# Kernel optimization log

Hardware: AMD Instinct MI355X
Metric: run time of the kernel (lower is better)

Reference implementation:

```python
import jax, jax.numpy as jnp
import numpy as np

N_NODES = 100000
N_EDGES = 1600000
DIMS = [64, 64, 64, 32]  # in -> hid -> hid -> out


def setup_inputs() -> dict:
    key = jax.random.key(0)
    ks = jax.random.split(key, 12)
    features = jax.random.normal(ks[0], (N_NODES, DIMS[0]), dtype=jnp.float32)
    edge_weights = jax.random.uniform(ks[1], (N_EDGES,), dtype=jnp.float32)
    src = jax.random.randint(ks[2], (N_EDGES,), 0, N_NODES, dtype=jnp.int32)
    dst = jax.random.randint(ks[3], (N_EDGES,), 0, N_NODES, dtype=jnp.int32)
    def lin(kw, kb, i, o):
        s = 1.0 / np.sqrt(i)
        W = jax.random.uniform(kw, (i, o), minval=-s, maxval=s, dtype=jnp.float32)
        b = jax.random.uniform(kb, (o,), minval=-s, maxval=s, dtype=jnp.float32)
        return W, b
    W1, b1 = lin(ks[4], ks[5], DIMS[0], DIMS[1])
    W2, b2 = lin(ks[6], ks[7], DIMS[1], DIMS[2])
    Wp, bp = lin(ks[8], ks[9], DIMS[2], DIMS[3])
    return {"features": features, "edge_weights": edge_weights, "src": src,
            "dst": dst, "W1": W1, "b1": b1, "W2": W2, "b2": b2,
            "Wp": Wp, "bp": bp}


def _graph_conv(x, src, dst, ew, W, b, norm_src, norm_dst):
    # DGL GraphConv, norm='both', with edge weights:
    # h = D_in^{-1/2} * A_w * (D_out^{-1/2} * x) @ W + b
    h = x * norm_src[:, None]
    msg = h[src] * ew[:, None]                      # [E, d] gather + edge-weight
    agg = jax.ops.segment_sum(msg, dst, num_segments=N_NODES)  # scatter-sum
    agg = agg * norm_dst[:, None]
    return agg @ W + b


def reference(features, edge_weights, src, dst, W1, b1, W2, b2, Wp, bp):
    ones = jnp.ones((N_EDGES,), dtype=features.dtype)
    out_deg = jax.ops.segment_sum(ones, src, num_segments=N_NODES)
    in_deg = jax.ops.segment_sum(ones, dst, num_segments=N_NODES)
    norm_src = jnp.power(jnp.clip(out_deg, 1.0, None), -0.5)
    norm_dst = jnp.power(jnp.clip(in_deg, 1.0, None), -0.5)

    x = jax.nn.relu(_graph_conv(features, src, dst, edge_weights, W1, b1, norm_src, norm_dst))
    x = jax.nn.relu(_graph_conv(x, src, dst, edge_weights, W2, b2, norm_src, norm_dst))
    x = _graph_conv(x, src, dst, edge_weights, Wp, bp, norm_src, norm_dst)
    return x
```

## Files before the change

### kernel.cpp

```cpp
#include <hip/hip_runtime.h>

#define N_NODES 100000
#define N_EDGES 1600000
#define NB_SCAN 391
#define NSLICE 64
#define SLICE_E 25000
#define NBUCK 4
#define BUCK_N 25000
#define BUCK_W 12500

__device__ __forceinline__ unsigned short f2bf(float f) {
    unsigned int u = __float_as_uint(f);
    return (unsigned short)((u + 0x7FFFu + ((u >> 16) & 1u)) >> 16);
}
__device__ __forceinline__ float bf2f(unsigned short b) {
    return __uint_as_float(((unsigned int)b) << 16);
}


template <bool RANK>
__global__ void __launch_bounds__(512) count_kernel(
        const int* __restrict__ ids,
        unsigned short* __restrict__ slicecnt,
        unsigned short* __restrict__ rank16) {
    __shared__ unsigned int cnt[BUCK_W];
    int s = blockIdx.x >> 2;
    int b = blockIdx.x & 3;
    int b0 = b * BUCK_N;
    for (int w = threadIdx.x; w < BUCK_W; w += 512) cnt[w] = 0;
    __syncthreads();
    int base = s * SLICE_E;
    for (int i = threadIdx.x; i < SLICE_E; i += 512) {
        int e = base + i;
        int id = ids[e] - b0;
        if ((unsigned)id < (unsigned)BUCK_N) {
            unsigned int shift = (id & 1) * 16;
            unsigned int old = atomicAdd(&cnt[id >> 1], 1u << shift);
            if (RANK) rank16[e] = (unsigned short)((old >> shift) & 0xFFFFu);
        }
    }
    __syncthreads();
    unsigned int* row = (unsigned int*)(slicecnt + (size_t)s * N_NODES) + b * BUCK_W;
    for (int w = threadIdx.x; w < BUCK_W; w += 512) row[w] = cnt[w];
}

__global__ void scan_slices_kernel(unsigned short* __restrict__ scd,
                                   const unsigned short* __restrict__ scs,
                                   int* __restrict__ deg_int,
                                   float* __restrict__ ndq,
                                   float* __restrict__ norm_src) {
    int n = blockIdx.x * blockDim.x + threadIdx.x;
    if (n >= N_NODES) return;
    unsigned int tot = 0;
    for (int s = 0; s < NSLICE; ++s) {
        size_t idx = (size_t)s * N_NODES + n;
        unsigned int c = scd[idx];
        scd[idx] = (unsigned short)tot;
        tot += c;
    }
    deg_int[n] = (int)tot;
    ndq[n] = rsqrtf(fmaxf((float)tot, 1.0f)) * (1.0f / 32767.0f);
    unsigned int so = 0;
    for (int s = 0; s < NSLICE; ++s) so += scs[(size_t)s * N_NODES + n];
    norm_src[n] = rsqrtf(fmaxf((float)so, 1.0f));
}


__global__ void block_sum_kernel(const int* __restrict__ deg_in, int* __restrict__ block_sums) {
    __shared__ int sdata[256];
    int t = threadIdx.x;
    int n = blockIdx.x * 256 + t;
    int v = (n < N_NODES) ? deg_in[n] : 0;
    sdata[t] = v;
    __syncthreads();
    for (int off = 128; off > 0; off >>= 1) {
        if (t < off) sdata[t] += sdata[t + off];
        __syncthreads();
    }
    if (t == 0) block_sums[blockIdx.x] = sdata[0];
}

__global__ void scan_blocks_kernel(const int* __restrict__ block_sums, int* __restrict__ block_off) {
    __shared__ int part[512];
    int t = threadIdx.x;
    int v = (t < NB_SCAN) ? block_sums[t] : 0;
    part[t] = v;
    __syncthreads();
    for (int off = 1; off < 512; off <<= 1) {
        int u = (t >= off) ? part[t - off] : 0;
        __syncthreads();
        part[t] += u;
        __syncthreads();
    }
    if (t < NB_SCAN) block_off[t] = part[t] - v;
}

__global__ void scatter_rowptr_kernel(const int* __restrict__ deg_in,
                                      const int* __restrict__ block_off,
                                      int* __restrict__ row_ptr) {
    __shared__ int part[256];
    int t = threadIdx.x;
    int n = blockIdx.x * 256 + t;
    int v = (n < N_NODES) ? deg_in[n] : 0;
    part[t] = v;
    __syncthreads();
    for (int off = 1; off < 256; off <<= 1) {
        int u = (t >= off) ? part[t - off] : 0;
        __syncthreads();
        part[t] += u;
        __syncthreads();
    }
    int excl = part[t] - v + block_off[blockIdx.x];
    if (n < N_NODES) row_ptr[n] = excl;
    if (n == N_NODES - 1) row_ptr[N_NODES] = excl + v;
}


__global__ void fill_kernel(const int* __restrict__ src, const int* __restrict__ dst,
                            const float* __restrict__ ew,
                            const int* __restrict__ row_ptr,
                            const unsigned short* __restrict__ sliceoff,
                            const unsigned short* __restrict__ rank16,
                            unsigned int* __restrict__ epack) {
    int i = blockIdx.x * blockDim.x + threadIdx.x;
    int stride = gridDim.x * blockDim.x;
    for (int e = i; e < N_EDGES; e += stride) {
        int s = src[e], d = dst[e];
        int sl = e / SLICE_E;
        int slot = row_ptr[d] + (int)sliceoff[(size_t)sl * N_NODES + d] + (int)rank16[e];
        unsigned int q = (unsigned int)(ew[e] * 32767.0f + 0.5f);
        epack[slot] = ((unsigned int)s << 15) | q;
    }
}


template <int BM, int DOUT, bool BIAS_RELU>
__global__ void __launch_bounds__(256) matmul_kernel(
        const float* __restrict__ x, const float* __restrict__ W,
        const float* __restrict__ bin, const float* __restrict__ ns,
        unsigned short* __restrict__ h) {
    constexpr int S = 65;
    constexpr int CG = DOUT / 4;
    __shared__ float Xs[BM * S];
    __shared__ float Ws[64 * DOUT];
    int tid = threadIdx.x;
    int n0 = blockIdx.x * BM;

    for (int i = tid; i < 16 * DOUT; i += 256)
        ((float4*)Ws)[i] = ((const float4*)W)[i];

    float4 bv4;
    if (BIAS_RELU) bv4 = ((const float4*)bin)[tid & 15];
    int c0 = (tid & 15) * 4;
    for (int r = tid >> 4; r < BM; r += 16) {
        int n = n0 + r;
        int nc = n < N_NODES ? n : N_NODES - 1;
        float4 v = ((const float4*)(x + (size_t)nc * 64))[tid & 15];
        if (BIAS_RELU) {
            v.x = fmaxf(v.x + bv4.x, 0.0f);
            v.y = fmaxf(v.y + bv4.y, 0.0f);
            v.z = fmaxf(v.z + bv4.z, 0.0f);
            v.w = fmaxf(v.w + bv4.w, 0.0f);
        }
        Xs[r * S + c0]     = v.x;
        Xs[r * S + c0 + 1] = v.y;
        Xs[r * S + c0 + 2] = v.z;
        Xs[r * S + c0 + 3] = v.w;
    }
    __syncthreads();

    int cg = tid % CG;
    int ng = tid / CG;
    float acc[4][4];
#pragma unroll
    for (int i = 0; i < 4; ++i)
#pragma unroll
        for (int j = 0; j < 4; ++j) acc[i][j] = 0.0f;

#pragma unroll 16
    for (int k = 0; k < 64; ++k) {
        float4 wk = *(const float4*)(&Ws[k * DOUT + cg * 4]);
        float xk[4];
#pragma unroll
        for (int i = 0; i < 4; ++i) xk[i] = Xs[(ng * 4 + i) * S + k];
#pragma unroll
        for (int i = 0; i < 4; ++i) {
            acc[i][0] = fmaf(xk[i], wk.x, acc[i][0]);
            acc[i][1] = fmaf(xk[i], wk.y, acc[i][1]);
            acc[i][2] = fmaf(xk[i], wk.z, acc[i][2]);
            acc[i][3] = fmaf(xk[i], wk.w, acc[i][3]);
        }
    }

#pragma unroll
    for (int i = 0; i < 4; ++i) {
        int n = n0 + ng * 4 + i;
        if (n < N_NODES) {
            float nsv = ns[n];
            ushort4 o;
            o.x = f2bf(acc[i][0] * nsv); o.y = f2bf(acc[i][1] * nsv);
            o.z = f2bf(acc[i][2] * nsv); o.w = f2bf(acc[i][3] * nsv);
            *(ushort4*)(&h[(size_t)n * DOUT + cg * 4]) = o;
        }
    }
}


template <int D, bool FINAL>
__global__ void __launch_bounds__(256) csr_agg_kernel(
        const int* __restrict__ row_ptr,
        const unsigned int* __restrict__ epack,
        const unsigned short* __restrict__ h,
        const float* __restrict__ ndq,
        const float* __restrict__ bias, float* __restrict__ out) {
    int tid = blockIdx.x * blockDim.x + threadIdx.x;
    int stride = gridDim.x * blockDim.x;
    int lane = threadIdx.x & (D - 1);
    int node0 = tid / D;
    int nstride = stride / D;
    const unsigned short* hl = h + lane;
    for (int n = node0; n < N_NODES; n += nstride) {
        int s = row_ptr[n];
        int e = row_ptr[n + 1];
        float a0 = 0.f, a1 = 0.f, a2 = 0.f, a3 = 0.f;
        float a4 = 0.f, a5 = 0.f, a6 = 0.f, a7 = 0.f;
        int i = s;
        for (; i + 7 < e; i += 8) {
            unsigned int p0 = epack[i],     p1 = epack[i + 1], p2 = epack[i + 2], p3 = epack[i + 3];
            unsigned int p4 = epack[i + 4], p5 = epack[i + 5], p6 = epack[i + 6], p7 = epack[i + 7];
            float h0 = bf2f(hl[(size_t)(p0 >> 15) * D]);
            float h1 = bf2f(hl[(size_t)(p1 >> 15) * D]);
            float h2 = bf2f(hl[(size_t)(p2 >> 15) * D]);
            float h3 = bf2f(hl[(size_t)(p3 >> 15) * D]);
            float h4 = bf2f(hl[(size_t)(p4 >> 15) * D]);
            float h5 = bf2f(hl[(size_t)(p5 >> 15) * D]);
            float h6 = bf2f(hl[(size_t)(p6 >> 15) * D]);
            float h7 = bf2f(hl[(size_t)(p7 >> 15) * D]);
            a0 = fmaf((float)(p0 & 32767u), h0, a0);
            a1 = fmaf((float)(p1 & 32767u), h1, a1);
            a2 = fmaf((float)(p2 & 32767u), h2, a2);
            a3 = fmaf((float)(p3 & 32767u), h3, a3);
            a4 = fmaf((float)(p4 & 32767u), h4, a4);
            a5 = fmaf((float)(p5 & 32767u), h5, a5);
            a6 = fmaf((float)(p6 & 32767u), h6, a6);
            a7 = fmaf((float)(p7 & 32767u), h7, a7);
        }
        for (; i + 3 < e; i += 4) {
            unsigned int p0 = epack[i], p1 = epack[i + 1], p2 = epack[i + 2], p3 = epack[i + 3];
            a0 = fmaf((float)(p0 & 32767u), bf2f(hl[(size_t)(p0 >> 15) * D]), a0);
            a1 = fmaf((float)(p1 & 32767u), bf2f(hl[(size_t)(p1 >> 15) * D]), a1);
            a2 = fmaf((float)(p2 & 32767u), bf2f(hl[(size_t)(p2 >> 15) * D]), a2);
            a3 = fmaf((float)(p3 & 32767u), bf2f(hl[(size_t)(p3 >> 15) * D]), a3);
        }
        for (; i < e; ++i) {
            unsigned int p = epack[i];
            a0 = fmaf((float)(p & 32767u), bf2f(hl[(size_t)(p >> 15) * D]), a0);
        }
        float acc = (((a0 + a1) + (a2 + a3)) + ((a4 + a5) + (a6 + a7))) * ndq[n];
        if (FINAL) out[(size_t)n * D + lane] = acc + bias[lane];
        else       out[(size_t)n * D + lane] = acc;
    }
}

extern "C" void kernel_launch(void* const* d_in, const int* in_sizes, int n_in,
                              void* d_out, int out_size, void* d_ws, size_t ws_size,
                              hipStream_t stream) {
    const float* features = (const float*)d_in[0];
    const float* ew       = (const float*)d_in[1];
    const int*   src      = (const int*)d_in[2];
    const int*   dst      = (const int*)d_in[3];
    const float* W1       = (const float*)d_in[4];
    const float* b1       = (const float*)d_in[5];
    const float* W2       = (const float*)d_in[6];
    const float* b2       = (const float*)d_in[7];
    const float* Wp       = (const float*)d_in[8];
    const float* bp       = (const float*)d_in[9];
    float* out = (float*)d_out;

    float* ws = (float*)d_ws;
    float* norm_src = ws;
    float* ndq      = ws + 100000;
    int*   deg_int  = (int*)(ws + 200000);
    int*   row_ptr  = (int*)(ws + 300000);
    int*   block_sums = (int*)(ws + 400002);
    int*   block_off  = (int*)(ws + 400394);
    unsigned short* rank16 = (unsigned short*)(ws + 400800);
    unsigned int*   epack  = (unsigned int*)(ws + 1200800);
    unsigned short* hbuf   = (unsigned short*)(ws + 2800800);
    float*          bufA   = ws + 6000800;

    unsigned short* slicecnt_dst = hbuf;
    unsigned short* slicecnt_src = (unsigned short*)bufA;

    count_kernel<true><<<NSLICE * NBUCK, 512, 0, stream>>>(dst, slicecnt_dst, rank16);
    count_kernel<false><<<NSLICE * NBUCK, 512, 0, stream>>>(src, slicecnt_src, nullptr);
    scan_slices_kernel<<<NB_SCAN, 256, 0, stream>>>(slicecnt_dst, slicecnt_src,
                                                    deg_int, ndq, norm_src);
    block_sum_kernel<<<NB_SCAN, 256, 0, stream>>>(deg_int, block_sums);
    scan_blocks_kernel<<<1, 512, 0, stream>>>(block_sums, block_off);
    scatter_rowptr_kernel<<<NB_SCAN, 256, 0, stream>>>(deg_int, block_off, row_ptr);
    fill_kernel<<<2048, 256, 0, stream>>>(src, dst, ew, row_ptr,
                                          slicecnt_dst, rank16, epack);

    matmul_kernel<64, 64, false><<<1563, 256, 0, stream>>>(features, W1, nullptr, norm_src, hbuf);
    csr_agg_kernel<64, false><<<4096, 256, 0, stream>>>(row_ptr, epack, hbuf, ndq, nullptr, bufA);

    matmul_kernel<64, 64, true><<<1563, 256, 0, stream>>>(bufA, W2, b1, norm_src, hbuf);
    csr_agg_kernel<64, false><<<4096, 256, 0, stream>>>(row_ptr, epack, hbuf, ndq, nullptr, bufA);

    matmul_kernel<128, 32, true><<<782, 256, 0, stream>>>(bufA, Wp, b2, norm_src, hbuf);
    csr_agg_kernel<32, true><<<4096, 256, 0, stream>>>(row_ptr, epack, hbuf, ndq, bp, out);
}
```

Before: 289.7 us.

## Assign one wavefront per node in CSR aggregation with packed bf16x2 loads

The CSR aggregation kernel now gives each 64-lane wavefront a single destination node. Lanes are split into groups that each handle a different edge, and every lane loads two bf16 features packed into one 32-bit word. Partial sums across edge groups are combined with shuffles, and lane group 0 writes a float2 result. This is meant to raise memory-level parallelism and widen the gathers for low-degree nodes, at the cost of cross-lane reductions and idle lanes in the tail loop.

```diff
diff --git a/kernel.cpp b/kernel.cpp
--- a/kernel.cpp
+++ b/kernel.cpp
@@ -12,9 +12,6 @@
 __device__ __forceinline__ unsigned short f2bf(float f) {
     unsigned int u = __float_as_uint(f);
     return (unsigned short)((u + 0x7FFFu + ((u >> 16) & 1u)) >> 16);
-}
-__device__ __forceinline__ float bf2f(unsigned short b) {
-    return __uint_as_float(((unsigned int)b) << 16);
 }
 
 
@@ -213,52 +210,71 @@
         const unsigned short* __restrict__ h,
         const float* __restrict__ ndq,
         const float* __restrict__ bias, float* __restrict__ out) {
+    constexpr int G = D / 2;
+    constexpr int EPL = 64 / G;
     int tid = blockIdx.x * blockDim.x + threadIdx.x;
-    int stride = gridDim.x * blockDim.x;
-    int lane = threadIdx.x & (D - 1);
-    int node0 = tid / D;
-    int nstride = stride / D;
-    const unsigned short* hl = h + lane;
-    for (int n = node0; n < N_NODES; n += nstride) {
+    int wave = tid >> 6;
+    int nwaves = (gridDim.x * blockDim.x) >> 6;
+    int lane = threadIdx.x & 63;
+    int grp = lane / G;
+    int j = lane % G;
+    const unsigned int* hw = (const unsigned int*)h;
+
+    float bx = 0.f, by = 0.f;
+    if (FINAL) { bx = bias[2 * j]; by = bias[2 * j + 1]; }
+
+    for (int n = wave; n < N_NODES; n += nwaves) {
         int s = row_ptr[n];
         int e = row_ptr[n + 1];
-        float a0 = 0.f, a1 = 0.f, a2 = 0.f, a3 = 0.f;
-        float a4 = 0.f, a5 = 0.f, a6 = 0.f, a7 = 0.f;
+        float ax0 = 0.f, ay0 = 0.f, ax1 = 0.f, ay1 = 0.f;
+        float ax2 = 0.f, ay2 = 0.f, ax3 = 0.f, ay3 = 0.f;
         int i = s;
-        for (; i + 7 < e; i += 8) {
-            unsigned int p0 = epack[i],     p1 = epack[i + 1], p2 = epack[i + 2], p3 = epack[i + 3];
-            unsigned int p4 = epack[i + 4], p5 = epack[i + 5], p6 = epack[i + 6], p7 = epack[i + 7];
-            float h0 = bf2f(hl[(size_t)(p0 >> 15) * D]);
-            float h1 = bf2f(hl[(size_t)(p1 >> 15) * D]);
-            float h2 = bf2f(hl[(size_t)(p2 >> 15) * D]);
-            float h3 = bf2f(hl[(size_t)(p3 >> 15) * D]);
-            float h4 = bf2f(hl[(size_t)(p4 >> 15) * D]);
-            float h5 = bf2f(hl[(size_t)(p5 >> 15) * D]);
-            float h6 = bf2f(hl[(size_t)(p6 >> 15) * D]);
-            float h7 = bf2f(hl[(size_t)(p7 >> 15) * D]);
-            a0 = fmaf((float)(p0 & 32767u), h0, a0);
-            a1 = fmaf((float)(p1 & 32767u), h1, a1);
-            a2 = fmaf((float)(p2 & 32767u), h2, a2);
-            a3 = fmaf((float)(p3 & 32767u), h3, a3);
-            a4 = fmaf((float)(p4 & 32767u), h4, a4);
-            a5 = fmaf((float)(p5 & 32767u), h5, a5);
-            a6 = fmaf((float)(p6 & 32767u), h6, a6);
-            a7 = fmaf((float)(p7 & 32767u), h7, a7);
-        }
-        for (; i + 3 < e; i += 4) {
-            unsigned int p0 = epack[i], p1 = epack[i + 1], p2 = epack[i + 2], p3 = epack[i + 3];
-            a0 = fmaf((float)(p0 & 32767u), bf2f(hl[(size_t)(p0 >> 15) * D]), a0);
-            a1 = fmaf((float)(p1 & 32767u), bf2f(hl[(size_t)(p1 >> 15) * D]), a1);
-            a2 = fmaf((float)(p2 & 32767u), bf2f(hl[(size_t)(p2 >> 15) * D]), a2);
-            a3 = fmaf((float)(p3 & 32767u), bf2f(hl[(size_t)(p3 >> 15) * D]), a3);
-        }
-        for (; i < e; ++i) {
-            unsigned int p = epack[i];
-            a0 = fmaf((float)(p & 32767u), bf2f(hl[(size_t)(p >> 15) * D]), a0);
-        }
-        float acc = (((a0 + a1) + (a2 + a3)) + ((a4 + a5) + (a6 + a7))) * ndq[n];
-        if (FINAL) out[(size_t)n * D + lane] = acc + bias[lane];
-        else       out[(size_t)n * D + lane] = acc;
+        for (; i + 4 * EPL <= e; i += 4 * EPL) {
+            unsigned int p0 = epack[i + grp];
+            unsigned int p1 = epack[i + EPL + grp];
+            unsigned int p2 = epack[i + 2 * EPL + grp];
+            unsigned int p3 = epack[i + 3 * EPL + grp];
+            unsigned int h0 = hw[(size_t)(p0 >> 15) * G + j];
+            unsigned int h1 = hw[(size_t)(p1 >> 15) * G + j];
+            unsigned int h2 = hw[(size_t)(p2 >> 15) * G + j];
+            unsigned int h3 = hw[(size_t)(p3 >> 15) * G + j];
+            float c0 = (float)(p0 & 32767u);
+            float c1 = (float)(p1 & 32767u);
+            float c2 = (float)(p2 & 32767u);
+            float c3 = (float)(p3 & 32767u);
+            ax0 = fmaf(__uint_as_float(h0 << 16), c0, ax0);
+            ay0 = fmaf(__uint_as_float(h0 & 0xFFFF0000u), c0, ay0);
+            ax1 = fmaf(__uint_as_float(h1 << 16), c1, ax1);
+            ay1 = fmaf(__uint_as_float(h1 & 0xFFFF0000u), c1, ay1);
+            ax2 = fmaf(__uint_as_float(h2 << 16), c2, ax2);
+            ay2 = fmaf(__uint_as_float(h2 & 0xFFFF0000u), c2, ay2);
+            ax3 = fmaf(__uint_as_float(h3 << 16), c3, ax3);
+            ay3 = fmaf(__uint_as_float(h3 & 0xFFFF0000u), c3, ay3);
+        }
+        for (; i < e; i += EPL) {
+            int idx = i + grp;
+            bool valid = idx < e;
+            unsigned int p = epack[valid ? idx : s];
+            unsigned int hv = hw[(size_t)(p >> 15) * G + j];
+            float c = valid ? (float)(p & 32767u) : 0.0f;
+            ax0 = fmaf(__uint_as_float(hv << 16), c, ax0);
+            ay0 = fmaf(__uint_as_float(hv & 0xFFFF0000u), c, ay0);
+        }
+        float sx = (ax0 + ax1) + (ax2 + ax3);
+        float sy = (ay0 + ay1) + (ay2 + ay3);
+        if (EPL == 4) {
+            sx += __shfl(sx, lane ^ 16);
+            sy += __shfl(sy, lane ^ 16);
+        }
+        sx += __shfl(sx, lane ^ 32);
+        sy += __shfl(sy, lane ^ 32);
+        if (grp == 0) {
+            float nv = ndq[n];
+            float2 o;
+            o.x = fmaf(sx, nv, bx);
+            o.y = fmaf(sy, nv, by);
+            *(float2*)(&out[(size_t)n * D + 2 * j]) = o;
+        }
     }
 }
 
```

New measurement: 294.5 us. No clear change (+1.6%).
